# Kernel tuning notes

Hardware: AMD Instinct MI355X
Metric: run time of the kernel (lower is better)

Reference implementation:

```python
import jax, jax.numpy as jnp
import numpy as np

EPS = 1e-5

def _layernorm(x, g, b):
    m = jnp.mean(x, axis=-1, keepdims=True)
    v = jnp.mean(jnp.square(x - m), axis=-1, keepdims=True)
    return (x - m) * jax.lax.rsqrt(v + EPS) * g + b

def setup_inputs() -> dict:
    key = jax.random.key(0)
    B, S, D, H = 2, 2048, 1024, 16
    F = 4 * D
    ks = jax.random.split(key, 12)
    s = 1.0 / np.sqrt(D)
    inp = {
        "x": jax.random.normal(ks[0], (B, S, D), dtype=jnp.float32),
        "mask": jnp.ones((B, S), dtype=jnp.int32),
        "wq": jax.random.normal(ks[1], (D, D), dtype=jnp.float32) * s,
        "bq": jnp.zeros((D,), jnp.float32),
        "wk": jax.random.normal(ks[2], (D, D), dtype=jnp.float32) * s,
        "bk": jnp.zeros((D,), jnp.float32),
        "wv": jax.random.normal(ks[3], (D, D), dtype=jnp.float32) * s,
        "bv": jnp.zeros((D,), jnp.float32),
        "wo": jax.random.normal(ks[4], (D, D), dtype=jnp.float32) * s,
        "bo": jnp.zeros((D,), jnp.float32),
        "g1": jnp.ones((D,), jnp.float32),
        "be1": jnp.zeros((D,), jnp.float32),
        "g2": jnp.ones((D,), jnp.float32),
        "be2": jnp.zeros((D,), jnp.float32),
        "w1": jax.random.normal(ks[5], (D, F), dtype=jnp.float32) * s,
        "bf1": jnp.zeros((F,), jnp.float32),
        "w2": jax.random.normal(ks[6], (F, D), dtype=jnp.float32) * (1.0 / np.sqrt(F)),
        "bf2": jnp.zeros((D,), jnp.float32),
    }
    return inp

def reference(x, mask, wq, bq, wk, bk, wv, bv, wo, bo, g1, be1, g2, be2, w1, bf1, w2, bf2):
    B, S, D = x.shape
    H = 16
    hd = D // H
    residual = x
    xn = _layernorm(x, g1, be1)
    q = (xn @ wq + bq).reshape(B, S, H, hd).transpose(0, 2, 1, 3)  # [B,H,S,hd]
    k = (xn @ wk + bk).reshape(B, S, H, hd).transpose(0, 2, 1, 3)
    v = (xn @ wv + bv).reshape(B, S, H, hd).transpose(0, 2, 1, 3)
    scores = jnp.einsum('bhqd,bhkd->bhqk', q, k) / np.sqrt(hd)  # [B,H,S,S]
    scores = jnp.where(mask[:, None, None, :] == 0, jnp.float32(-1e9), scores)
    attn = jax.nn.softmax(scores, axis=-1)
    attended = jnp.einsum('bhqk,bhkd->bhqd', attn, v)
    attended = attended.transpose(0, 2, 1, 3).reshape(B, S, D)
    x = residual + (attended @ wo + bo)
    residual = x
    xn = _layernorm(x, g2, be2)
    ff = jax.nn.relu(xn @ w1 + bf1) @ w2 + bf2
    return residual + ff
```

## Files before the change

### kernel.cpp

```cpp
#include <hip/hip_runtime.h>
#include <hip/hip_bf16.h>


using bf16 = __hip_bfloat16;
typedef short bf16x8 __attribute__((ext_vector_type(8)));
typedef short bf16x4v __attribute__((ext_vector_type(4)));
typedef float f32x4 __attribute__((ext_vector_type(4)));

#if defined(__has_builtin)
#  if __has_builtin(__builtin_amdgcn_mfma_f32_16x16x16bf16_1k)
#    define HAVE_MFMA_K16 1
#  endif
#endif

__device__ __forceinline__ float toF(float v) { return v; }
__device__ __forceinline__ float toF(bf16 v) { return __bfloat162float(v); }
__device__ __forceinline__ void storeF(float* p, float v) { *p = v; }
__device__ __forceinline__ void storeF(bf16* p, float v) { *p = __float2bfloat16(v); }

__device__ __forceinline__ float waveReduceSum(float v) {
    #pragma unroll
    for (int o = 32; o > 0; o >>= 1) v += __shfl_down(v, o, 64);
    return v;
}

__device__ __forceinline__ void async16(const bf16* g, bf16* l) {
    __builtin_amdgcn_global_load_lds(
        (const __attribute__((address_space(1))) unsigned int*)g,
        (__attribute__((address_space(3))) unsigned int*)l,
        16, 0, 0);
}

__device__ __forceinline__ unsigned short bf16bits(float x) {
    union { bf16 h; unsigned short u; } e; e.h = __float2bfloat16(x);
    return e.u;
}

__global__ __launch_bounds__(256) void transpose_cast(const float* __restrict__ in,
                                                      bf16* __restrict__ outT,
                                                      int R, int C) {
    __shared__ float t[32][33];
    const int c0 = blockIdx.x * 32, r0 = blockIdx.y * 32;
    const int lx = threadIdx.x & 31, ly = threadIdx.x >> 5;
    #pragma unroll
    for (int i = 0; i < 32; i += 8)
        t[ly + i][lx] = in[(size_t)(r0 + ly + i) * C + c0 + lx];
    __syncthreads();
    #pragma unroll
    for (int i = 0; i < 32; i += 8)
        outT[(size_t)(c0 + ly + i) * R + r0 + lx] = __float2bfloat16(t[lx][ly + i]);
}

template <typename InT>
__global__ __launch_bounds__(256) void ln_kernel(const InT* __restrict__ x,
                                                 const float* __restrict__ g,
                                                 const float* __restrict__ b,
                                                 bf16* __restrict__ out, int D) {
    const int row = blockIdx.x;
    const InT* xr = x + (size_t)row * D;
    float s = 0.f, s2 = 0.f;
    for (int i = threadIdx.x; i < D; i += 256) {
        float v = toF(xr[i]);
        s += v; s2 += v * v;
    }
    __shared__ float ws[4], ws2[4];
    int lane = threadIdx.x & 63, wid = threadIdx.x >> 6;
    s = waveReduceSum(s); s2 = waveReduceSum(s2);
    if (lane == 0) { ws[wid] = s; ws2[wid] = s2; }
    __syncthreads();
    float ts = ws[0] + ws[1] + ws[2] + ws[3];
    float ts2 = ws2[0] + ws2[1] + ws2[2] + ws2[3];
    float mean = ts / D;
    float var = ts2 / D - mean * mean;
    float rstd = rsqrtf(var + 1e-5f);
    bf16* outr = out + (size_t)row * D;
    for (int i = threadIdx.x; i < D; i += 256) {
        float v = (toF(xr[i]) - mean) * rstd * g[i] + b[i];
        outr[i] = __float2bfloat16(v);
    }
}

template <int BM, typename OutT, typename ResidT, bool RELU, bool HAS_RESID, bool BIAS3>
__global__ __launch_bounds__(256) void gemm_mfma(const bf16* __restrict__ A,
                                                 const bf16* __restrict__ BT,
                                                 const float* __restrict__ bias,
                                                 const float* __restrict__ biasK,
                                                 const float* __restrict__ biasV,
                                                 const ResidT* __restrict__ resid,
                                                 OutT* __restrict__ C,
                                                 int M, int N, int K) {
    constexpr int BK = 32;
    constexpr int MI = BM / 32;
    __shared__ bf16 As[BM][BK];
    __shared__ bf16 Bs[128][BK];
    const int tid = threadIdx.x, lane = tid & 63, wid = tid >> 6;
    const int m0 = blockIdx.y * BM, n0 = blockIdx.x * 128;
    const int wm = (BM == 128) ? (wid >> 1) * 64 : (wid & 1) * 32;
    const int wn = (BM == 128) ? (wid & 1) * 64 : (wid >> 1) * 64;

    f32x4 acc[MI][4] = {};

    const int srow = wid * 16 + (lane >> 2);
    const int scol = (lane & 3) * 8;
    const size_t aBase0 = (size_t)(m0 + srow) * K + scol;
    const size_t aBase1 = (size_t)(m0 + (BM == 128 ? 64 : 0) + srow) * K + scol;
    const size_t bBase0 = (size_t)(n0 + srow) * K + scol;
    const size_t bBase1 = (size_t)(n0 + 64 + srow) * K + scol;

    const int fr = lane & 15;
    const int fk = (lane >> 4) * 8;

    for (int k0 = 0; k0 < K; k0 += BK) {
        async16(A + aBase0 + k0, &As[wid * 16][0]);
        if (BM == 128)
            async16(A + aBase1 + k0, &As[(BM == 128 ? 64 : 0) + wid * 16][0]);
        async16(BT + bBase0 + k0, &Bs[wid * 16][0]);
        async16(BT + bBase1 + k0, &Bs[64 + wid * 16][0]);
        __syncthreads();

        bf16x8 aF[MI], bF[4];
        #pragma unroll
        for (int i = 0; i < MI; ++i)
            aF[i] = *(const bf16x8*)&As[wm + i * 16 + fr][fk];
        #pragma unroll
        for (int j = 0; j < 4; ++j)
            bF[j] = *(const bf16x8*)&Bs[wn + j * 16 + fr][fk];
        #pragma unroll
        for (int i = 0; i < MI; ++i)
            #pragma unroll
            for (int j = 0; j < 4; ++j)
                acc[i][j] = __builtin_amdgcn_mfma_f32_16x16x32_bf16(
                    aF[i], bF[j], acc[i][j], 0, 0, 0);
        __syncthreads();
    }

    const int col_l = lane & 15, row_l = (lane >> 4) * 4;
    #pragma unroll
    for (int j = 0; j < 4; ++j) {
        const int col = n0 + wn + j * 16 + col_l;
        float bvv;
        if (BIAS3) {
            const float* bp = (col < 1024) ? bias : ((col < 2048) ? biasK : biasV);
            bvv = bp[col & 1023];
        } else {
            bvv = bias[col];
        }
        #pragma unroll
        for (int i = 0; i < MI; ++i) {
            #pragma unroll
            for (int r = 0; r < 4; ++r) {
                const int row = m0 + wm + i * 16 + row_l + r;
                float v = acc[i][j][r] + bvv;
                if (RELU) v = fmaxf(v, 0.f);
                if (HAS_RESID) v += toF(resid[(size_t)row * N + col]);
                storeF(&C[(size_t)row * N + col], v);
            }
        }
    }
}

#if HAVE_MFMA_K16
__global__ __launch_bounds__(256) void attn_mfma(const bf16* __restrict__ qkv,
                                                 const int* __restrict__ mask,
                                                 bf16* __restrict__ outp,
                                                 int B, int S, int LD) {
    const int q0 = blockIdx.x * 64;
    const int h = blockIdx.y, b = blockIdx.z;
    const int Do = 1024;
    const int tid = threadIdx.x, lane = tid & 63, wid = tid >> 6;
    const int n = lane & 15, kg = lane >> 4;

    __shared__ bf16 Ks[64][66];
    __shared__ bf16 Vt[64][68];
    __shared__ float Mskf[64];

    bf16x8 qf[2];
    {
        const bf16* qp = qkv + ((size_t)(b * S + q0 + wid * 16 + n)) * LD + h * 64 + kg * 8;
        union { uint4 u; bf16x8 v; unsigned short s[8]; } c[2];
        c[0].u = *(const uint4*)qp;
        c[1].u = *(const uint4*)(qp + 32);
        #pragma unroll
        for (int t = 0; t < 2; ++t) {
            #pragma unroll
            for (int i = 0; i < 8; ++i) {
                union { float f; unsigned int u; } d;
                d.u = ((unsigned int)c[t].s[i]) << 16;
                c[t].s[i] = bf16bits(d.f * 0.125f);
            }
            qf[t] = c[t].v;
        }
    }

    f32x4 acc_o[4] = {};
    float m = -1e30f, l = 0.f;

    const int sr = tid >> 2, sc = (tid & 3) * 16;
    const int jp = tid & 31, dg = (tid >> 5) * 8;
    const bf16* kbase = qkv + (size_t)(b * S) * LD + 1024 + h * 64;
    const bf16* vbase = qkv + (size_t)(b * S) * LD + 2048 + h * 64;

    for (int j0 = 0; j0 < S; j0 += 64) {
        __syncthreads();
        {
            const bf16* kp = kbase + (size_t)(j0 + sr) * LD + sc;
            uint4 ka = *(const uint4*)kp;
            uint4 kc = *(const uint4*)(kp + 8);
            uint* kd = (uint*)((char*)&Ks[0][0] + sr * 132 + sc * 2);
            kd[0] = ka.x; kd[1] = ka.y; kd[2] = ka.z; kd[3] = ka.w;
            kd[4] = kc.x; kd[5] = kc.y; kd[6] = kc.z; kd[7] = kc.w;

            const bf16* vp = vbase + (size_t)(j0 + 2 * jp) * LD + dg;
            union { uint4 u; unsigned short s[8]; } va, vc;
            va.u = *(const uint4*)vp;
            vc.u = *(const uint4*)(vp + LD);
            #pragma unroll
            for (int i = 0; i < 8; ++i) {
                unsigned int pk = (unsigned int)va.s[i] | ((unsigned int)vc.s[i] << 16);
                *(unsigned int*)((char*)&Vt[0][0] + (size_t)(dg + i) * 136 + jp * 4) = pk;
            }
            if (tid < 64) Mskf[tid] = (mask[b * S + j0 + tid] == 0) ? -1e9f : 0.f;
        }
        __syncthreads();

        f32x4 st[4] = {};
        #pragma unroll
        for (int ks = 0; ks < 2; ++ks) {
            #pragma unroll
            for (int jt = 0; jt < 4; ++jt) {
                union { uint u[4]; bf16x8 v; } kf;
                const uint* bp = (const uint*)((const char*)&Ks[0][0]
                                 + (size_t)(jt * 16 + n) * 132 + ks * 64 + kg * 16);
                kf.u[0] = bp[0]; kf.u[1] = bp[1]; kf.u[2] = bp[2]; kf.u[3] = bp[3];
                st[jt] = __builtin_amdgcn_mfma_f32_16x16x32_bf16(kf.v, qf[ks], st[jt], 0, 0, 0);
            }
        }

        float mx = m;
        #pragma unroll
        for (int jt = 0; jt < 4; ++jt) {
            f32x4 mb = *(const f32x4*)&Mskf[jt * 16 + kg * 4];
            #pragma unroll
            for (int r = 0; r < 4; ++r) {
                st[jt][r] += mb[r];
                mx = fmaxf(mx, st[jt][r]);
            }
        }
        mx = fmaxf(mx, __shfl_xor(mx, 16, 64));
        mx = fmaxf(mx, __shfl_xor(mx, 32, 64));
        float alpha = __expf(m - mx);
        m = mx;
        float ls = 0.f;
        bf16x4v pf[4];
        #pragma unroll
        for (int jt = 0; jt < 4; ++jt) {
            union { unsigned short s[4]; bf16x4v v; } pk;
            #pragma unroll
            for (int r = 0; r < 4; ++r) {
                float p = __expf(st[jt][r] - m);
                ls += p;
                pk.s[r] = bf16bits(p);
            }
            pf[jt] = pk.v;
        }
        ls += __shfl_xor(ls, 16, 64);
        ls += __shfl_xor(ls, 32, 64);
        l = l * alpha + ls;
        #pragma unroll
        for (int dt = 0; dt < 4; ++dt)
            #pragma unroll
            for (int r = 0; r < 4; ++r) acc_o[dt][r] *= alpha;

        #pragma unroll
        for (int jt = 0; jt < 4; ++jt) {
            #pragma unroll
            for (int dt = 0; dt < 4; ++dt) {
                union { uint u[2]; bf16x4v v; } vf;
                const uint* vpp = (const uint*)((const char*)&Vt[0][0]
                                  + (size_t)(dt * 16 + n) * 136 + jt * 32 + kg * 8);
                vf.u[0] = vpp[0]; vf.u[1] = vpp[1];
                acc_o[dt] = __builtin_amdgcn_mfma_f32_16x16x16bf16_1k(
                    vf.v, pf[jt], acc_o[dt], 0, 0, 0);
            }
        }
    }

    float inv = (l > 0.f) ? (1.f / l) : 0.f;
    bf16* op = outp + ((size_t)(b * S + q0 + wid * 16 + n)) * Do + h * 64;
    #pragma unroll
    for (int dt = 0; dt < 4; ++dt) {
        union { unsigned short s[4]; uint2 u; } w;
        #pragma unroll
        for (int r = 0; r < 4; ++r) w.s[r] = bf16bits(acc_o[dt][r] * inv);
        *(uint2*)(op + dt * 16 + kg * 4) = w.u;
    }
}
#else
__global__ __launch_bounds__(256) void attn_mfma(const bf16* __restrict__ qkv,
                                                 const int* __restrict__ mask,
                                                 bf16* __restrict__ outp,
                                                 int B, int S, int LD) {
    const int q0 = blockIdx.x * 64;
    const int h = blockIdx.y, b = blockIdx.z;
    const int Do = 1024;
    const int tid = threadIdx.x, lane = tid & 63, wid = tid >> 6;
    const int n = lane & 15, kg = lane >> 4;

    __shared__ bf16 Ks[64][66];
    __shared__ bf16 Vt[64][66];
    __shared__ bf16 Plds[4][16][66];
    __shared__ int  Msk[64];

    bf16x8 qf[2];
    {
        const bf16* qp = qkv + ((size_t)(b * S + q0 + wid * 16 + n)) * LD + h * 64 + kg * 8;
        union { uint4 u; bf16x8 v; } c0, c1;
        c0.u = *(const uint4*)qp;
        c1.u = *(const uint4*)(qp + 32);
        qf[0] = c0.v; qf[1] = c1.v;
    }

    f32x4 acc_o[4] = {};
    float m_r[4] = {-1e30f, -1e30f, -1e30f, -1e30f};
    float l_r[4] = {0.f, 0.f, 0.f, 0.f};

    const int sr = tid >> 2;
    const int sc = (tid & 3) * 16;
    const bf16* kbase = qkv + (size_t)(b * S) * LD + 1024 + h * 64;
    const bf16* vbase = qkv + (size_t)(b * S) * LD + 2048 + h * 64;

    for (int j0 = 0; j0 < S; j0 += 64) {
        __syncthreads();
        {
            const bf16* kp = kbase + (size_t)(j0 + sr) * LD + sc;
            uint4 ka = *(const uint4*)kp;
            uint4 kbv = *(const uint4*)(kp + 8);
            uint* kd = (uint*)((char*)&Ks[0][0] + sr * 132 + sc * 2);
            kd[0] = ka.x; kd[1] = ka.y; kd[2] = ka.z; kd[3] = ka.w;
            kd[4] = kbv.x; kd[5] = kbv.y; kd[6] = kbv.z; kd[7] = kbv.w;

            const bf16* vp = vbase + (size_t)(j0 + sr) * LD + sc;
            union { uint4 u[2]; unsigned short s[16]; } vv;
            vv.u[0] = *(const uint4*)vp;
            vv.u[1] = *(const uint4*)(vp + 8);
            #pragma unroll
            for (int i = 0; i < 16; ++i)
                *((unsigned short*)((char*)&Vt[0][0] + (size_t)(sc + i) * 132 + sr * 2)) = vv.s[i];

            if (tid < 64) Msk[tid] = mask[b * S + j0 + tid];
        }
        __syncthreads();

        f32x4 st[4] = {};
        #pragma unroll
        for (int ks = 0; ks < 2; ++ks) {
            #pragma unroll
            for (int jt = 0; jt < 4; ++jt) {
                union { uint u[4]; bf16x8 v; } bf;
                const uint* bp = (const uint*)((const char*)&Ks[0][0]
                                 + (size_t)(jt * 16 + n) * 132 + ks * 64 + kg * 16);
                bf.u[0] = bp[0]; bf.u[1] = bp[1]; bf.u[2] = bp[2]; bf.u[3] = bp[3];
                st[jt] = __builtin_amdgcn_mfma_f32_16x16x32_bf16(qf[ks], bf.v, st[jt], 0, 0, 0);
            }
        }

        int mk[4];
        #pragma unroll
        for (int jt = 0; jt < 4; ++jt) mk[jt] = Msk[jt * 16 + n];

        #pragma unroll
        for (int r = 0; r < 4; ++r) {
            float mx = -1e30f;
            #pragma unroll
            for (int jt = 0; jt < 4; ++jt) {
                float s = st[jt][r] * 0.125f;
                if (mk[jt] == 0) s = -1e9f;
                st[jt][r] = s;
                mx = fmaxf(mx, s);
            }
            #pragma unroll
            for (int o = 1; o < 16; o <<= 1) mx = fmaxf(mx, __shfl_xor(mx, o, 64));
            float newm = fmaxf(m_r[r], mx);
            float alpha = __expf(m_r[r] - newm);
            m_r[r] = newm;
            float ls = 0.f;
            #pragma unroll
            for (int jt = 0; jt < 4; ++jt) {
                float p = __expf(st[jt][r] - newm);
                ls += p;
                Plds[wid][kg * 4 + r][jt * 16 + n] = __float2bfloat16(p);
            }
            #pragma unroll
            for (int o = 1; o < 16; o <<= 1) ls += __shfl_xor(ls, o, 64);
            l_r[r] = l_r[r] * alpha + ls;
            #pragma unroll
            for (int dt = 0; dt < 4; ++dt) acc_o[dt][r] *= alpha;
        }

        __asm__ volatile("s_waitcnt lgkmcnt(0)" ::: "memory");

        #pragma unroll
        for (int ks = 0; ks < 2; ++ks) {
            union { uint u[4]; bf16x8 v; } af;
            const uint* ap = (const uint*)((const char*)&Plds[wid][0][0]
                             + (size_t)n * 132 + ks * 64 + kg * 16);
            af.u[0] = ap[0]; af.u[1] = ap[1]; af.u[2] = ap[2]; af.u[3] = ap[3];
            #pragma unroll
            for (int dt = 0; dt < 4; ++dt) {
                union { uint u[4]; bf16x8 v; } bf;
                const uint* bp = (const uint*)((const char*)&Vt[0][0]
                                 + (size_t)(dt * 16 + n) * 132 + ks * 64 + kg * 16);
                bf.u[0] = bp[0]; bf.u[1] = bp[1]; bf.u[2] = bp[2]; bf.u[3] = bp[3];
                acc_o[dt] = __builtin_amdgcn_mfma_f32_16x16x32_bf16(af.v, bf.v, acc_o[dt], 0, 0, 0);
            }
        }
    }

    #pragma unroll
    for (int r = 0; r < 4; ++r) {
        float inv = (l_r[r] > 0.f) ? (1.f / l_r[r]) : 0.f;
        bf16* op = outp + ((size_t)(b * S + q0 + wid * 16 + kg * 4 + r)) * Do + h * 64 + n;
        #pragma unroll
        for (int dt = 0; dt < 4; ++dt)
            op[dt * 16] = __float2bfloat16(acc_o[dt][r] * inv);
    }
}
#endif

extern "C" void kernel_launch(void* const* d_in, const int* in_sizes, int n_in,
                              void* d_out, int out_size, void* d_ws, size_t ws_size,
                              hipStream_t stream) {
    const int B = 2, S = 2048, D = 1024, H = 16, F = 4096;
    const int M = B * S;

    const float* x   = (const float*)d_in[0];
    const int*   mask= (const int*)  d_in[1];
    const float* wq  = (const float*)d_in[2];
    const float* bq  = (const float*)d_in[3];
    const float* wk  = (const float*)d_in[4];
    const float* bk  = (const float*)d_in[5];
    const float* wv  = (const float*)d_in[6];
    const float* bv  = (const float*)d_in[7];
    const float* wo  = (const float*)d_in[8];
    const float* bo  = (const float*)d_in[9];
    const float* g1  = (const float*)d_in[10];
    const float* be1 = (const float*)d_in[11];
    const float* g2  = (const float*)d_in[12];
    const float* be2 = (const float*)d_in[13];
    const float* w1  = (const float*)d_in[14];
    const float* bf1 = (const float*)d_in[15];
    const float* w2  = (const float*)d_in[16];
    const float* bf2 = (const float*)d_in[17];
    float* out = (float*)d_out;

    char* ws = (char*)d_ws;
    const size_t MB = 1024 * 1024;
    bf16* wqkvT = (bf16*)(ws + 0 * MB);
    bf16* woT   = (bf16*)(ws + 6 * MB);
    bf16* w1T   = (bf16*)(ws + 8 * MB);
    bf16* w2T   = (bf16*)(ws + 16 * MB);
    bf16* xn    = (bf16*)(ws + 24 * MB);
    bf16* qkv   = (bf16*)(ws + 32 * MB);
    bf16* att   = xn;

    const bool fullM = (ws_size >= 64 * MB);

    transpose_cast<<<dim3(D / 32, D / 32), 256, 0, stream>>>(wq, wqkvT, D, D);
    transpose_cast<<<dim3(D / 32, D / 32), 256, 0, stream>>>(wk, wqkvT + (size_t)1024 * 1024, D, D);
    transpose_cast<<<dim3(D / 32, D / 32), 256, 0, stream>>>(wv, wqkvT + (size_t)2048 * 1024, D, D);
    transpose_cast<<<dim3(D / 32, D / 32), 256, 0, stream>>>(wo, woT, D, D);
    transpose_cast<<<dim3(F / 32, D / 32), 256, 0, stream>>>(w1, w1T, D, F);
    transpose_cast<<<dim3(D / 32, F / 32), 256, 0, stream>>>(w2, w2T, F, D);

    ln_kernel<float><<<M, 256, 0, stream>>>(x, g1, be1, xn, D);

    gemm_mfma<128, bf16, float, false, false, true><<<dim3(3072 / 128, M / 128), 256, 0, stream>>>(
        xn, wqkvT, bq, bk, bv, (const float*)nullptr, qkv, M, 3072, D);

    attn_mfma<<<dim3(S / 64, H, B), 256, 0, stream>>>(qkv, mask, att, B, S, 3072);

    gemm_mfma<64, float, float, false, true, false><<<dim3(D / 128, M / 64), 256, 0, stream>>>(
        att, woT, bo, nullptr, nullptr, x, out, M, D, D);

    if (fullM) {
        bf16* hid = (bf16*)(ws + 24 * MB);
        bf16* xn2 = (bf16*)(ws + 56 * MB);
        ln_kernel<float><<<M, 256, 0, stream>>>(out, g2, be2, xn2, D);
        gemm_mfma<128, bf16, float, true, false, false><<<dim3(F / 128, M / 128), 256, 0, stream>>>(
            xn2, w1T, bf1, nullptr, nullptr, (const float*)nullptr, hid, M, F, D);
        gemm_mfma<64, float, float, false, true, false><<<dim3(D / 128, M / 64), 256, 0, stream>>>(
            hid, w2T, bf2, nullptr, nullptr, out, out, M, D, F);
    } else {
        bf16* xn2 = (bf16*)(ws + 32 * MB);
        bf16* hid = (bf16*)(ws + 40 * MB);
        const int CH = 2048;
        ln_kernel<float><<<M, 256, 0, stream>>>(out, g2, be2, xn2, D);
        for (int c = 0; c < M / CH; ++c) {
            const size_t roff = (size_t)c * CH;
            gemm_mfma<128, bf16, float, true, false, false><<<dim3(F / 128, CH / 128), 256, 0, stream>>>(
                xn2 + roff * D, w1T, bf1, nullptr, nullptr, (const float*)nullptr, hid, CH, F, D);
            gemm_mfma<64, float, float, false, true, false><<<dim3(D / 128, CH / 64), 256, 0, stream>>>(
                hid, w2T, bf2, nullptr, nullptr, out + roff * D, out + roff * D, CH, D, F);
        }
    }
}
```

Baseline: 443.4 us.

## Process 128 queries per attention block and merge weight transposes into one launch

The MFMA attention kernel now has each wave handle two 16-row query tiles, so a block covers 128 queries and each K/V tile staged in shared memory is reused twice. This halves K/V global loads and LDS staging per query, at the cost of more registers and half as many blocks (512), which may lower occupancy. Separately, the six weight transpose-cast launches are folded into one kernel that picks its segment from blockIdx, removing launch overhead. The fallback attention path loops over two 64-query halves to match the new grid.

After: 429.9 us. -3.0%, faster.

```diff
diff --git a/kernel.cpp b/kernel.cpp
--- a/kernel.cpp
+++ b/kernel.cpp
@@ -36,11 +36,26 @@
     return e.u;
 }
 
-__global__ __launch_bounds__(256) void transpose_cast(const float* __restrict__ in,
-                                                      bf16* __restrict__ outT,
-                                                      int R, int C) {
+__global__ __launch_bounds__(256) void transpose_all(
+        const float* __restrict__ wq, const float* __restrict__ wk,
+        const float* __restrict__ wv, const float* __restrict__ wo,
+        const float* __restrict__ w1, const float* __restrict__ w2,
+        bf16* __restrict__ wqkvT, bf16* __restrict__ woT,
+        bf16* __restrict__ w1T, bf16* __restrict__ w2T) {
     __shared__ float t[32][33];
-    const int c0 = blockIdx.x * 32, r0 = blockIdx.y * 32;
+    const int tI = blockIdx.x;
+    const float* in; bf16* outT; int R, C, tl;
+    if (tI < 4096) {
+        const int seg = tI >> 10; tl = tI & 1023; R = 1024; C = 1024;
+        in = (seg == 0) ? wq : (seg == 1) ? wk : (seg == 2) ? wv : wo;
+        outT = (seg == 3) ? woT : wqkvT + (size_t)seg * 1024 * 1024;
+    } else if (tI < 8192) {
+        tl = tI - 4096; in = w1; outT = w1T; R = 1024; C = 4096;
+    } else {
+        tl = tI - 8192; in = w2; outT = w2T; R = 4096; C = 1024;
+    }
+    const int tc = C >> 5;
+    const int c0 = (tl % tc) * 32, r0 = (tl / tc) * 32;
     const int lx = threadIdx.x & 31, ly = threadIdx.x >> 5;
     #pragma unroll
     for (int i = 0; i < 32; i += 8)
@@ -164,7 +179,7 @@
                                                  const int* __restrict__ mask,
                                                  bf16* __restrict__ outp,
                                                  int B, int S, int LD) {
-    const int q0 = blockIdx.x * 64;
+    const int q0 = blockIdx.x * 128;
     const int h = blockIdx.y, b = blockIdx.z;
     const int Do = 1024;
     const int tid = threadIdx.x, lane = tid & 63, wid = tid >> 6;
@@ -174,26 +189,27 @@
     __shared__ bf16 Vt[64][68];
     __shared__ float Mskf[64];
 
-    bf16x8 qf[2];
-    {
-        const bf16* qp = qkv + ((size_t)(b * S + q0 + wid * 16 + n)) * LD + h * 64 + kg * 8;
-        union { uint4 u; bf16x8 v; unsigned short s[8]; } c[2];
-        c[0].u = *(const uint4*)qp;
-        c[1].u = *(const uint4*)(qp + 32);
+    bf16x8 qf[2][2];
+    #pragma unroll
+    for (int u = 0; u < 2; ++u) {
+        const bf16* qp = qkv + ((size_t)(b * S + q0 + wid * 32 + u * 16 + n)) * LD + h * 64 + kg * 8;
+        union { uint4 uu; bf16x8 v; unsigned short s[8]; } c[2];
+        c[0].uu = *(const uint4*)qp;
+        c[1].uu = *(const uint4*)(qp + 32);
         #pragma unroll
         for (int t = 0; t < 2; ++t) {
             #pragma unroll
             for (int i = 0; i < 8; ++i) {
-                union { float f; unsigned int u; } d;
-                d.u = ((unsigned int)c[t].s[i]) << 16;
+                union { float f; unsigned int u2; } d;
+                d.u2 = ((unsigned int)c[t].s[i]) << 16;
                 c[t].s[i] = bf16bits(d.f * 0.125f);
             }
-            qf[t] = c[t].v;
-        }
-    }
-
-    f32x4 acc_o[4] = {};
-    float m = -1e30f, l = 0.f;
+            qf[u][t] = c[t].v;
+        }
+    }
+
+    f32x4 acc[2][4] = {};
+    float m[2] = {-1e30f, -1e30f}, l[2] = {0.f, 0.f};
 
     const int sr = tid >> 2, sc = (tid & 3) * 16;
     const int jp = tid & 31, dg = (tid >> 5) * 8;
@@ -223,7 +239,7 @@
         }
         __syncthreads();
 
-        f32x4 st[4] = {};
+        f32x4 st[2][4] = {};
         #pragma unroll
         for (int ks = 0; ks < 2; ++ks) {
             #pragma unroll
@@ -232,44 +248,48 @@
                 const uint* bp = (const uint*)((const char*)&Ks[0][0]
                                  + (size_t)(jt * 16 + n) * 132 + ks * 64 + kg * 16);
                 kf.u[0] = bp[0]; kf.u[1] = bp[1]; kf.u[2] = bp[2]; kf.u[3] = bp[3];
-                st[jt] = __builtin_amdgcn_mfma_f32_16x16x32_bf16(kf.v, qf[ks], st[jt], 0, 0, 0);
-            }
-        }
-
-        float mx = m;
-        #pragma unroll
-        for (int jt = 0; jt < 4; ++jt) {
-            f32x4 mb = *(const f32x4*)&Mskf[jt * 16 + kg * 4];
-            #pragma unroll
-            for (int r = 0; r < 4; ++r) {
-                st[jt][r] += mb[r];
-                mx = fmaxf(mx, st[jt][r]);
-            }
-        }
-        mx = fmaxf(mx, __shfl_xor(mx, 16, 64));
-        mx = fmaxf(mx, __shfl_xor(mx, 32, 64));
-        float alpha = __expf(m - mx);
-        m = mx;
-        float ls = 0.f;
-        bf16x4v pf[4];
-        #pragma unroll
-        for (int jt = 0; jt < 4; ++jt) {
-            union { unsigned short s[4]; bf16x4v v; } pk;
-            #pragma unroll
-            for (int r = 0; r < 4; ++r) {
-                float p = __expf(st[jt][r] - m);
-                ls += p;
-                pk.s[r] = bf16bits(p);
-            }
-            pf[jt] = pk.v;
-        }
-        ls += __shfl_xor(ls, 16, 64);
-        ls += __shfl_xor(ls, 32, 64);
-        l = l * alpha + ls;
-        #pragma unroll
-        for (int dt = 0; dt < 4; ++dt)
-            #pragma unroll
-            for (int r = 0; r < 4; ++r) acc_o[dt][r] *= alpha;
+                st[0][jt] = __builtin_amdgcn_mfma_f32_16x16x32_bf16(kf.v, qf[0][ks], st[0][jt], 0, 0, 0);
+                st[1][jt] = __builtin_amdgcn_mfma_f32_16x16x32_bf16(kf.v, qf[1][ks], st[1][jt], 0, 0, 0);
+            }
+        }
+
+        bf16x4v pf[2][4];
+        #pragma unroll
+        for (int u = 0; u < 2; ++u) {
+            float mx = m[u];
+            #pragma unroll
+            for (int jt = 0; jt < 4; ++jt) {
+                f32x4 mb = *(const f32x4*)&Mskf[jt * 16 + kg * 4];
+                #pragma unroll
+                for (int r = 0; r < 4; ++r) {
+                    st[u][jt][r] += mb[r];
+                    mx = fmaxf(mx, st[u][jt][r]);
+                }
+            }
+            mx = fmaxf(mx, __shfl_xor(mx, 16, 64));
+            mx = fmaxf(mx, __shfl_xor(mx, 32, 64));
+            float alpha = __expf(m[u] - mx);
+            m[u] = mx;
+            float ls = 0.f;
+            #pragma unroll
+            for (int jt = 0; jt < 4; ++jt) {
+                union { unsigned short s[4]; bf16x4v v; } pk;
+                #pragma unroll
+                for (int r = 0; r < 4; ++r) {
+                    float p = __expf(st[u][jt][r] - mx);
+                    ls += p;
+                    pk.s[r] = bf16bits(p);
+                }
+                pf[u][jt] = pk.v;
+            }
+            ls += __shfl_xor(ls, 16, 64);
+            ls += __shfl_xor(ls, 32, 64);
+            l[u] = l[u] * alpha + ls;
+            #pragma unroll
+            for (int dt = 0; dt < 4; ++dt)
+                #pragma unroll
+                for (int r = 0; r < 4; ++r) acc[u][dt][r] *= alpha;
+        }
 
         #pragma unroll
         for (int jt = 0; jt < 4; ++jt) {
@@ -279,20 +299,23 @@
                 const uint* vpp = (const uint*)((const char*)&Vt[0][0]
                                   + (size_t)(dt * 16 + n) * 136 + jt * 32 + kg * 8);
                 vf.u[0] = vpp[0]; vf.u[1] = vpp[1];
-                acc_o[dt] = __builtin_amdgcn_mfma_f32_16x16x16bf16_1k(
-                    vf.v, pf[jt], acc_o[dt], 0, 0, 0);
-            }
-        }
-    }
-
-    float inv = (l > 0.f) ? (1.f / l) : 0.f;
-    bf16* op = outp + ((size_t)(b * S + q0 + wid * 16 + n)) * Do + h * 64;
+                acc[0][dt] = __builtin_amdgcn_mfma_f32_16x16x16bf16_1k(vf.v, pf[0][jt], acc[0][dt], 0, 0, 0);
+                acc[1][dt] = __builtin_amdgcn_mfma_f32_16x16x16bf16_1k(vf.v, pf[1][jt], acc[1][dt], 0, 0, 0);
+            }
+        }
+    }
+
     #pragma unroll
-    for (int dt = 0; dt < 4; ++dt) {
-        union { unsigned short s[4]; uint2 u; } w;
-        #pragma unroll
-        for (int r = 0; r < 4; ++r) w.s[r] = bf16bits(acc_o[dt][r] * inv);
-        *(uint2*)(op + dt * 16 + kg * 4) = w.u;
+    for (int u = 0; u < 2; ++u) {
+        float inv = (l[u] > 0.f) ? (1.f / l[u]) : 0.f;
+        bf16* op = outp + ((size_t)(b * S + q0 + wid * 32 + u * 16 + n)) * Do + h * 64;
+        #pragma unroll
+        for (int dt = 0; dt < 4; ++dt) {
+            union { unsigned short s[4]; uint2 u2; } w;
+            #pragma unroll
+            for (int r = 0; r < 4; ++r) w.s[r] = bf16bits(acc[u][dt][r] * inv);
+            *(uint2*)(op + dt * 16 + kg * 4) = w.u2;
+        }
     }
 }
 #else
@@ -300,7 +323,6 @@
                                                  const int* __restrict__ mask,
                                                  bf16* __restrict__ outp,
                                                  int B, int S, int LD) {
-    const int q0 = blockIdx.x * 64;
     const int h = blockIdx.y, b = blockIdx.z;
     const int Do = 1024;
     const int tid = threadIdx.x, lane = tid & 63, wid = tid >> 6;
@@ -311,118 +333,123 @@
     __shared__ bf16 Plds[4][16][66];
     __shared__ int  Msk[64];
 
-    bf16x8 qf[2];
-    {
-        const bf16* qp = qkv + ((size_t)(b * S + q0 + wid * 16 + n)) * LD + h * 64 + kg * 8;
-        union { uint4 u; bf16x8 v; } c0, c1;
-        c0.u = *(const uint4*)qp;
-        c1.u = *(const uint4*)(qp + 32);
-        qf[0] = c0.v; qf[1] = c1.v;
-    }
-
-    f32x4 acc_o[4] = {};
-    float m_r[4] = {-1e30f, -1e30f, -1e30f, -1e30f};
-    float l_r[4] = {0.f, 0.f, 0.f, 0.f};
-
-    const int sr = tid >> 2;
-    const int sc = (tid & 3) * 16;
-    const bf16* kbase = qkv + (size_t)(b * S) * LD + 1024 + h * 64;
-    const bf16* vbase = qkv + (size_t)(b * S) * LD + 2048 + h * 64;
-
-    for (int j0 = 0; j0 < S; j0 += 64) {
+    for (int half = 0; half < 2; ++half) {
+        const int q0 = blockIdx.x * 128 + half * 64;
         __syncthreads();
+
+        bf16x8 qf[2];
         {
-            const bf16* kp = kbase + (size_t)(j0 + sr) * LD + sc;
-            uint4 ka = *(const uint4*)kp;
-            uint4 kbv = *(const uint4*)(kp + 8);
-            uint* kd = (uint*)((char*)&Ks[0][0] + sr * 132 + sc * 2);
-            kd[0] = ka.x; kd[1] = ka.y; kd[2] = ka.z; kd[3] = ka.w;
-            kd[4] = kbv.x; kd[5] = kbv.y; kd[6] = kbv.z; kd[7] = kbv.w;
-
-            const bf16* vp = vbase + (size_t)(j0 + sr) * LD + sc;
-            union { uint4 u[2]; unsigned short s[16]; } vv;
-            vv.u[0] = *(const uint4*)vp;
-            vv.u[1] = *(const uint4*)(vp + 8);
-            #pragma unroll
-            for (int i = 0; i < 16; ++i)
-                *((unsigned short*)((char*)&Vt[0][0] + (size_t)(sc + i) * 132 + sr * 2)) = vv.s[i];
-
-            if (tid < 64) Msk[tid] = mask[b * S + j0 + tid];
-        }
-        __syncthreads();
-
-        f32x4 st[4] = {};
-        #pragma unroll
-        for (int ks = 0; ks < 2; ++ks) {
-            #pragma unroll
-            for (int jt = 0; jt < 4; ++jt) {
-                union { uint u[4]; bf16x8 v; } bf;
-                const uint* bp = (const uint*)((const char*)&Ks[0][0]
-                                 + (size_t)(jt * 16 + n) * 132 + ks * 64 + kg * 16);
-                bf.u[0] = bp[0]; bf.u[1] = bp[1]; bf.u[2] = bp[2]; bf.u[3] = bp[3];
-                st[jt] = __builtin_amdgcn_mfma_f32_16x16x32_bf16(qf[ks], bf.v, st[jt], 0, 0, 0);
-            }
-        }
-
-        int mk[4];
-        #pragma unroll
-        for (int jt = 0; jt < 4; ++jt) mk[jt] = Msk[jt * 16 + n];
+            const bf16* qp = qkv + ((size_t)(b * S + q0 + wid * 16 + n)) * LD + h * 64 + kg * 8;
+            union { uint4 u; bf16x8 v; } c0, c1;
+            c0.u = *(const uint4*)qp;
+            c1.u = *(const uint4*)(qp + 32);
+            qf[0] = c0.v; qf[1] = c1.v;
+        }
+
+        f32x4 acc_o[4] = {};
+        float m_r[4] = {-1e30f, -1e30f, -1e30f, -1e30f};
+        float l_r[4] = {0.f, 0.f, 0.f, 0.f};
+
+        const int sr = tid >> 2;
+        const int sc = (tid & 3) * 16;
+        const bf16* kbase = qkv + (size_t)(b * S) * LD + 1024 + h * 64;
+        const bf16* vbase = qkv + (size_t)(b * S) * LD + 2048 + h * 64;
+
+        for (int j0 = 0; j0 < S; j0 += 64) {
+            __syncthreads();
+            {
+                const bf16* kp = kbase + (size_t)(j0 + sr) * LD + sc;
+                uint4 ka = *(const uint4*)kp;
+                uint4 kbv = *(const uint4*)(kp + 8);
+                uint* kd = (uint*)((char*)&Ks[0][0] + sr * 132 + sc * 2);
+                kd[0] = ka.x; kd[1] = ka.y; kd[2] = ka.z; kd[3] = ka.w;
+                kd[4] = kbv.x; kd[5] = kbv.y; kd[6] = kbv.z; kd[7] = kbv.w;
+
+                const bf16* vp = vbase + (size_t)(j0 + sr) * LD + sc;
+                union { uint4 u[2]; unsigned short s[16]; } vv;
+                vv.u[0] = *(const uint4*)vp;
+                vv.u[1] = *(const uint4*)(vp + 8);
+                #pragma unroll
+                for (int i = 0; i < 16; ++i)
+                    *((unsigned short*)((char*)&Vt[0][0] + (size_t)(sc + i) * 132 + sr * 2)) = vv.s[i];
+
+                if (tid < 64) Msk[tid] = mask[b * S + j0 + tid];
+            }
+            __syncthreads();
+
+            f32x4 st[4] = {};
+            #pragma unroll
+            for (int ks = 0; ks < 2; ++ks) {
+                #pragma unroll
+                for (int jt = 0; jt < 4; ++jt) {
+                    union { uint u[4]; bf16x8 v; } bf;
+                    const uint* bp = (const uint*)((const char*)&Ks[0][0]
+                                     + (size_t)(jt * 16 + n) * 132 + ks * 64 + kg * 16);
+                    bf.u[0] = bp[0]; bf.u[1] = bp[1]; bf.u[2] = bp[2]; bf.u[3] = bp[3];
+                    st[jt] = __builtin_amdgcn_mfma_f32_16x16x32_bf16(qf[ks], bf.v, st[jt], 0, 0, 0);
+                }
+            }
+
+            int mk[4];
+            #pragma unroll
+            for (int jt = 0; jt < 4; ++jt) mk[jt] = Msk[jt * 16 + n];
+
+            #pragma unroll
+            for (int r = 0; r < 4; ++r) {
+                float mx = -1e30f;
+                #pragma unroll
+                for (int jt = 0; jt < 4; ++jt) {
+                    float s = st[jt][r] * 0.125f;
+                    if (mk[jt] == 0) s = -1e9f;
+                    st[jt][r] = s;
+                    mx = fmaxf(mx, s);
+                }
+                #pragma unroll
+                for (int o = 1; o < 16; o <<= 1) mx = fmaxf(mx, __shfl_xor(mx, o, 64));
+                float newm = fmaxf(m_r[r], mx);
+                float alpha = __expf(m_r[r] - newm);
+                m_r[r] = newm;
+                float ls = 0.f;
+                #pragma unroll
+                for (int jt = 0; jt < 4; ++jt) {
+                    float p = __expf(st[jt][r] - newm);
+                    ls += p;
+                    Plds[wid][kg * 4 + r][jt * 16 + n] = __float2bfloat16(p);
+                }
+                #pragma unroll
+                for (int o = 1; o < 16; o <<= 1) ls += __shfl_xor(ls, o, 64);
+                l_r[r] = l_r[r] * alpha + ls;
+                #pragma unroll
+                for (int dt = 0; dt < 4; ++dt) acc_o[dt][r] *= alpha;
+            }
+
+            __asm__ volatile("s_waitcnt lgkmcnt(0)" ::: "memory");
+
+            #pragma unroll
+            for (int ks = 0; ks < 2; ++ks) {
+                union { uint u[4]; bf16x8 v; } af;
+                const uint* ap = (const uint*)((const char*)&Plds[wid][0][0]
+                                 + (size_t)n * 132 + ks * 64 + kg * 16);
+                af.u[0] = ap[0]; af.u[1] = ap[1]; af.u[2] = ap[2]; af.u[3] = ap[3];
+                #pragma unroll
+                for (int dt = 0; dt < 4; ++dt) {
+                    union { uint u[4]; bf16x8 v; } bf;
+                    const uint* bp = (const uint*)((const char*)&Vt[0][0]
+                                     + (size_t)(dt * 16 + n) * 132 + ks * 64 + kg * 16);
+                    bf.u[0] = bp[0]; bf.u[1] = bp[1]; bf.u[2] = bp[2]; bf.u[3] = bp[3];
+                    acc_o[dt] = __builtin_amdgcn_mfma_f32_16x16x32_bf16(af.v, bf.v, acc_o[dt], 0, 0, 0);
+                }
+            }
+        }
 
         #pragma unroll
         for (int r = 0; r < 4; ++r) {
-            float mx = -1e30f;
-            #pragma unroll
-            for (int jt = 0; jt < 4; ++jt) {
-                float s = st[jt][r] * 0.125f;
-                if (mk[jt] == 0) s = -1e9f;
-                st[jt][r] = s;
-                mx = fmaxf(mx, s);
-            }
-            #pragma unroll
-            for (int o = 1; o < 16; o <<= 1) mx = fmaxf(mx, __shfl_xor(mx, o, 64));
-            float newm = fmaxf(m_r[r], mx);
-            float alpha = __expf(m_r[r] - newm);
-            m_r[r] = newm;
-            float ls = 0.f;
-            #pragma unroll
-            for (int jt = 0; jt < 4; ++jt) {
-                float p = __expf(st[jt][r] - newm);
-                ls += p;
-                Plds[wid][kg * 4 + r][jt * 16 + n] = __float2bfloat16(p);
-            }
-            #pragma unroll
-            for (int o = 1; o < 16; o <<= 1) ls += __shfl_xor(ls, o, 64);
-            l_r[r] = l_r[r] * alpha + ls;
-            #pragma unroll
-            for (int dt = 0; dt < 4; ++dt) acc_o[dt][r] *= alpha;
-        }
-
-        __asm__ volatile("s_waitcnt lgkmcnt(0)" ::: "memory");
-
-        #pragma unroll
-        for (int ks = 0; ks < 2; ++ks) {
-            union { uint u[4]; bf16x8 v; } af;
-            const uint* ap = (const uint*)((const char*)&Plds[wid][0][0]
-                             + (size_t)n * 132 + ks * 64 + kg * 16);
-            af.u[0] = ap[0]; af.u[1] = ap[1]; af.u[2] = ap[2]; af.u[3] = ap[3];
-            #pragma unroll
-            for (int dt = 0; dt < 4; ++dt) {
-                union { uint u[4]; bf16x8 v; } bf;
-                const uint* bp = (const uint*)((const char*)&Vt[0][0]
-                                 + (size_t)(dt * 16 + n) * 132 + ks * 64 + kg * 16);
-                bf.u[0] = bp[0]; bf.u[1] = bp[1]; bf.u[2] = bp[2]; bf.u[3] = bp[3];
-                acc_o[dt] = __builtin_amdgcn_mfma_f32_16x16x32_bf16(af.v, bf.v, acc_o[dt], 0, 0, 0);
-            }
-        }
-    }
-
-    #pragma unroll
-    for (int r = 0; r < 4; ++r) {
-        float inv = (l_r[r] > 0.f) ? (1.f / l_r[r]) : 0.f;
-        bf16* op = outp + ((size_t)(b * S + q0 + wid * 16 + kg * 4 + r)) * Do + h * 64 + n;
-        #pragma unroll
-        for (int dt = 0; dt < 4; ++dt)
-            op[dt * 16] = __float2bfloat16(acc_o[dt][r] * inv);
+            float inv = (l_r[r] > 0.f) ? (1.f / l_r[r]) : 0.f;
+            bf16* op = outp + ((size_t)(b * S + q0 + wid * 16 + kg * 4 + r)) * Do + h * 64 + n;
+            #pragma unroll
+            for (int dt = 0; dt < 4; ++dt)
+                op[dt * 16] = __float2bfloat16(acc_o[dt][r] * inv);
+        }
     }
 }
 #endif
@@ -465,19 +492,15 @@
 
     const bool fullM = (ws_size >= 64 * MB);
 
-    transpose_cast<<<dim3(D / 32, D / 32), 256, 0, stream>>>(wq, wqkvT, D, D);
-    transpose_cast<<<dim3(D / 32, D / 32), 256, 0, stream>>>(wk, wqkvT + (size_t)1024 * 1024, D, D);
-    transpose_cast<<<dim3(D / 32, D / 32), 256, 0, stream>>>(wv, wqkvT + (size_t)2048 * 1024, D, D);
-    transpose_cast<<<dim3(D / 32, D / 32), 256, 0, stream>>>(wo, woT, D, D);
-    transpose_cast<<<dim3(F / 32, D / 32), 256, 0, stream>>>(w1, w1T, D, F);
-    transpose_cast<<<dim3(D / 32, F / 32), 256, 0, stream>>>(w2, w2T, F, D);
+    transpose_all<<<12288, 256, 0, stream>>>(wq, wk, wv, wo, w1, w2,
+                                             wqkvT, woT, w1T, w2T);
 
     ln_kernel<float><<<M, 256, 0, stream>>>(x, g1, be1, xn, D);
 
     gemm_mfma<128, bf16, float, false, false, true><<<dim3(3072 / 128, M / 128), 256, 0, stream>>>(
         xn, wqkvT, bq, bk, bv, (const float*)nullptr, qkv, M, 3072, D);
 
-    attn_mfma<<<dim3(S / 64, H, B), 256, 0, stream>>>(qkv, mask, att, B, S, 3072);
+    attn_mfma<<<dim3(S / 128, H, B), 256, 0, stream>>>(qkv, mask, att, B, S, 3072);
 
     gemm_mfma<64, float, float, false, true, false><<<dim3(D / 128, M / 64), 256, 0, stream>>>(
         att, woT, bo, nullptr, nullptr, x, out, M, D, D);
```
